# Kernel tuning notes

Measured on AMD Instinct MI355X. Metric: run time of the kernel, lower is better.

## Reference

```python
import jax, jax.numpy as jnp
import numpy as np

N_NODES = 100000
N_EDGES = 3200000
D_FEAT = 256
GC_HID = 20      # CVAEEncoder.hidden_dim default
DEC_HID = 40     # CVAEDecoder.hidden_dim default
Z_DIM = 32
EXPR_DIM = 256
SIGMA_BOUND = 0.0001


def setup_inputs() -> dict:
    key = jax.random.key(0)
    ks = jax.random.split(key, 16)
    inp = {
        "nodes": jax.random.normal(ks[0], (N_NODES, D_FEAT), dtype=jnp.float32),
        "senders": jax.random.randint(ks[1], (N_EDGES,), 0, N_NODES, dtype=jnp.int32),
        "receivers": jax.random.randint(ks[2], (N_EDGES,), 0, N_NODES, dtype=jnp.int32),
        "eps": jax.random.normal(ks[3], (N_NODES, Z_DIM), dtype=jnp.float32),
    }
    def dense(k, fan_in, fan_out):
        # flax default: lecun_normal kernel, zero bias
        w = jax.random.normal(k, (fan_in, fan_out), dtype=jnp.float32) / np.sqrt(fan_in)
        return w, jnp.zeros((fan_out,), jnp.float32)
    inp["W_gc1"], inp["b_gc1"] = dense(ks[4], D_FEAT, GC_HID)
    inp["W_gc2"], inp["b_gc2"] = dense(ks[5], GC_HID, GC_HID)
    inp["W_mu"], inp["b_mu"] = dense(ks[6], GC_HID + D_FEAT, Z_DIM)
    inp["W_ls"], inp["b_ls"] = dense(ks[7], GC_HID + D_FEAT, Z_DIM)
    inp["W_d1"], inp["b_d1"] = dense(ks[8], Z_DIM, DEC_HID)
    inp["W_d2"], inp["b_d2"] = dense(ks[9], DEC_HID, EXPR_DIM)
    return inp


def _gcn_layer(h, senders, receivers, W, b):
    # jraph.GraphConvolution: update_node_fn = softmax(relu(Dense(x))),
    # then symmetric-normalized segment_sum aggregation (no self edges).
    h = jax.nn.softmax(jax.nn.relu(h @ W + b), axis=-1)  # [N, GC_HID]
    ones = jnp.ones(senders.shape, h.dtype)
    deg_s = jax.ops.segment_sum(ones, senders, N_NODES)
    deg_r = jax.ops.segment_sum(ones, receivers, N_NODES)
    h = h * jax.lax.rsqrt(jnp.maximum(deg_s, 1.0))[:, None]
    h = jax.ops.segment_sum(h[senders], receivers, N_NODES)  # irregular gather+scatter
    h = h * jax.lax.rsqrt(jnp.maximum(deg_r, 1.0))[:, None]
    return h


def reference(nodes, senders, receivers, eps,
              W_gc1, b_gc1, W_gc2, b_gc2,
              W_mu, b_mu, W_ls, b_ls,
              W_d1, b_d1, W_d2, b_d2):
    # Encoder: 2 GC layers
    h = _gcn_layer(nodes, senders, receivers, W_gc1, b_gc1)
    h = _gcn_layer(h, senders, receivers, W_gc2, b_gc2)
    h = jnp.concatenate([h, nodes], axis=-1)  # [N, GC_HID + D_FEAT]
    mu = h @ W_mu + b_mu
    logsig2 = h @ W_ls + b_ls
    # Reparameterization
    sigma = SIGMA_BOUND + jnp.exp(0.5 * logsig2)
    z = mu + sigma * eps
    # Decoder MLP (nlayers=2 -> one hidden relu layer)
    d = jax.nn.relu(z @ W_d1 + b_d1)
    Xsample = d @ W_d2 + b_d2
    return Xsample, mu, logsig2
```

## Files before the change

kernel.cpp:

```cpp
#include <hip/hip_runtime.h>
#include <math.h>

#define N_NODES 100000
#define N_EDGES 3200000
#define D_FEAT 256
#define GC_HID 20
#define DEC_HID 40
#define Z_DIM 32

#define EPB 2048
#define NBLK 1563
#define SB 392
#define SBSH 8
#define S2CAP 12288


__device__ inline unsigned short f2bf(float f) {
    unsigned u = __float_as_uint(f);
    return (unsigned short)((u + 0x7FFFu + ((u >> 16) & 1u)) >> 16);
}
__device__ inline float bf2f(unsigned short h) {
    return __uint_as_float((unsigned)h << 16);
}
__device__ inline float bflo(unsigned w) { return __uint_as_float(w << 16); }
__device__ inline float bfhi(unsigned w) { return __uint_as_float(w & 0xFFFF0000u); }

__global__ __launch_bounds__(96) void k_wpack(const float* __restrict__ W1,
                                              const float* __restrict__ Wmu,
                                              const float* __restrict__ Wls,
                                              float* __restrict__ Wp) {
    int k = blockIdx.x, j = threadIdx.x;
    float v = 0.0f;
    if (j < 20) v = W1[k * GC_HID + j];
    else if (j >= 24 && j < 56) v = Wmu[(GC_HID + k) * Z_DIM + (j - 24)];
    else if (j >= 56 && j < 88) v = Wls[(GC_HID + k) * Z_DIM + (j - 56)];
    Wp[k * 96 + j] = v;
}

__global__ __launch_bounds__(512) void k_sort(const int* __restrict__ snd,
                                              const int* __restrict__ rcv,
                                              unsigned* __restrict__ rec_r,
                                              unsigned char* __restrict__ rec_s,
                                              unsigned short* __restrict__ srow_r,
                                              unsigned short* __restrict__ srow_s) {
    __shared__ int es[EPB], er[EPB];
    __shared__ unsigned scan[SB + 1];
    __shared__ unsigned cur[SB];
    __shared__ unsigned sorted[EPB];
    __shared__ unsigned char sorteds[EPB];
    int b = blockIdx.x, t = threadIdx.x;
    int base = b * EPB;
    int cnt = min(EPB, N_EDGES - base);
    for (int i = t; i < cnt; i += 512) { es[i] = snd[base + i]; er[i] = rcv[base + i]; }

    for (int i = t; i < SB + 1; i += 512) scan[i] = 0u;
    __syncthreads();
    for (int i = t; i < cnt; i += 512) atomicAdd(&scan[(er[i] >> SBSH) + 1], 1u);
    __syncthreads();
    for (int off = 1; off < SB + 1; off <<= 1) {
        unsigned v = (t >= off && t < SB + 1) ? scan[t - off] : 0u;
        __syncthreads();
        if (t < SB + 1) scan[t] += v;
        __syncthreads();
    }
    for (int i = t; i < SB + 1; i += 512) srow_r[(size_t)b * (SB + 1) + i] = (unsigned short)scan[i];
    if (t < SB) cur[t] = scan[t];
    __syncthreads();
    for (int i = t; i < cnt; i += 512) {
        int r = er[i];
        unsigned pos = atomicAdd(&cur[r >> SBSH], 1u);
        sorted[pos] = ((unsigned)(r & 255) << 17) | (unsigned)es[i];
    }
    __syncthreads();
    for (int i = t; i < cnt; i += 512) rec_r[(size_t)base + i] = sorted[i];
    __syncthreads();

    for (int i = t; i < SB + 1; i += 512) scan[i] = 0u;
    __syncthreads();
    for (int i = t; i < cnt; i += 512) atomicAdd(&scan[(es[i] >> SBSH) + 1], 1u);
    __syncthreads();
    for (int off = 1; off < SB + 1; off <<= 1) {
        unsigned v = (t >= off && t < SB + 1) ? scan[t - off] : 0u;
        __syncthreads();
        if (t < SB + 1) scan[t] += v;
        __syncthreads();
    }
    for (int i = t; i < SB + 1; i += 512) srow_s[(size_t)b * (SB + 1) + i] = (unsigned short)scan[i];
    if (t < SB) cur[t] = scan[t];
    __syncthreads();
    for (int i = t; i < cnt; i += 512) {
        int s = es[i];
        unsigned pos = atomicAdd(&cur[s >> SBSH], 1u);
        sorteds[pos] = (unsigned char)(s & 255);
    }
    __syncthreads();
    for (int i = t; i < cnt; i += 512) rec_s[(size_t)base + i] = sorteds[i];
}

__global__ __launch_bounds__(512) void k_degs(const unsigned char* __restrict__ rec_s,
                                              const unsigned short* __restrict__ srow_s,
                                              float* __restrict__ rs_s) {
    __shared__ unsigned h[256];
    int s = blockIdx.x, t = threadIdx.x;
    if (t < 256) h[t] = 0u;
    __syncthreads();
    for (int k = t; k < NBLK; k += 512) {
        const unsigned short* row = srow_s + (size_t)k * (SB + 1);
        unsigned st = row[s], en = row[s + 1];
        const unsigned char* rp = rec_s + (size_t)k * EPB;
        for (unsigned i = st; i < en; ++i) atomicAdd(&h[rp[i]], 1u);
    }
    __syncthreads();
    if (t < 256) {
        int n = (s << SBSH) + t;
        if (n < N_NODES) rs_s[n] = rsqrtf(fmaxf((float)h[t], 1.0f));
    }
}

__global__ __launch_bounds__(256) void k_scanB(const unsigned short* __restrict__ srow_r,
                                               unsigned* __restrict__ pref_t,
                                               unsigned* __restrict__ gtot) {
    __shared__ unsigned buf[256];
    int s = blockIdx.x, t = threadIdx.x;
    unsigned run = 0;
    for (int k0 = 0; k0 < NBLK; k0 += 256) {
        int k = k0 + t;
        unsigned v = 0;
        if (k < NBLK) {
            const unsigned short* row = srow_r + (size_t)k * (SB + 1);
            v = (unsigned)row[s + 1] - (unsigned)row[s];
        }
        buf[t] = v;
        __syncthreads();
        for (int off = 1; off < 256; off <<= 1) {
            unsigned x = (t >= off) ? buf[t - off] : 0u;
            __syncthreads();
            buf[t] += x;
            __syncthreads();
        }
        if (k < NBLK) pref_t[(size_t)s * NBLK + k] = run + (buf[t] - v);
        unsigned tot = buf[255];
        __syncthreads();
        run += tot;
    }
    if (t == 0) gtot[s] = run;
}

__global__ __launch_bounds__(512) void k_scanG(const unsigned* __restrict__ gtot,
                                               unsigned* __restrict__ gbase) {
    __shared__ unsigned buf[SB];
    int t = threadIdx.x;
    if (t < SB) buf[t] = gtot[t];
    __syncthreads();
    for (int off = 1; off < SB; off <<= 1) {
        unsigned x = (t >= off && t < SB) ? buf[t - off] : 0u;
        __syncthreads();
        if (t < SB) buf[t] += x;
        __syncthreads();
    }
    if (t < SB) gbase[t + 1] = buf[t];
    if (t == 0) gbase[0] = 0u;
}

__global__ __launch_bounds__(256) void k_gscat(const unsigned* __restrict__ rec_r,
                                               const unsigned short* __restrict__ srow_r,
                                               const unsigned* __restrict__ pref_t,
                                               const unsigned* __restrict__ gbase,
                                               unsigned* __restrict__ grec) {
    __shared__ unsigned recs[EPB];
    __shared__ unsigned short srow[SB + 1];
    int b = blockIdx.x, t = threadIdx.x;
    int base = b * EPB;
    int cnt = min(EPB, N_EDGES - base);
    for (int i = t; i < cnt; i += 256) recs[i] = rec_r[(size_t)base + i];
    for (int i = t; i < SB + 1; i += 256) srow[i] = srow_r[(size_t)b * (SB + 1) + i];
    __syncthreads();
    for (int s = t; s < SB; s += 256) {
        unsigned lo = srow[s], hi = srow[s + 1];
        if (lo == hi) continue;
        unsigned dst = gbase[s] + pref_t[(size_t)s * NBLK + b];
        for (unsigned i = lo; i < hi; ++i) grec[dst + (i - lo)] = recs[i];
    }
}

__global__ __launch_bounds__(256) void k_sort2(unsigned* __restrict__ grec,
                                               const unsigned* __restrict__ gbase,
                                               unsigned* __restrict__ row_ptr) {
    __shared__ unsigned recs[S2CAP];
    __shared__ unsigned hist[256];
    __shared__ unsigned scan[256];
    __shared__ unsigned cur[256];
    int s = blockIdx.x, t = threadIdx.x;
    unsigned lo = gbase[s], hi = gbase[s + 1];
    unsigned cnt = min(hi - lo, (unsigned)S2CAP);
    for (unsigned i = t; i < cnt; i += 256) recs[i] = grec[lo + i];
    hist[t] = 0u;
    __syncthreads();
    for (unsigned i = t; i < cnt; i += 256) atomicAdd(&hist[recs[i] >> 17], 1u);
    __syncthreads();
    unsigned v = hist[t];
    scan[t] = v;
    __syncthreads();
    for (int off = 1; off < 256; off <<= 1) {
        unsigned x = (t >= off) ? scan[t - off] : 0u;
        __syncthreads();
        scan[t] += x;
        __syncthreads();
    }
    unsigned excl = scan[t] - v;
    {
        int n = (s << SBSH) + t;
        if (n <= N_NODES) row_ptr[n] = lo + excl;
    }
    cur[t] = excl;
    __syncthreads();
    for (unsigned i = t; i < cnt; i += 256) {
        unsigned rec = recs[i];
        unsigned pos = atomicAdd(&cur[rec >> 17], 1u);
        grec[lo + pos] = rec & 0x1FFFFu;
    }
}

__global__ __launch_bounds__(320) void k_gg1(const unsigned* __restrict__ row_ptr,
                                             const unsigned* __restrict__ grec,
                                             const unsigned* __restrict__ src,
                                             const float* __restrict__ W2,
                                             const float* __restrict__ b2,
                                             const float* __restrict__ rs_s,
                                             unsigned short* __restrict__ h2_pre) {
    __shared__ float h1[64 * 21];
    __shared__ float Wsh[GC_HID * GC_HID];
    __shared__ float bsh[GC_HID];
    int t = threadIdx.x;
    if (t < GC_HID * GC_HID) Wsh[t] = W2[t];
    if (t >= 400 && t < 400 + GC_HID) bsh[t - 400] = b2[t - 400];
    int nl = t / 5, q = t % 5;
    int node = blockIdx.x * 64 + nl;
    bool live = (node < N_NODES);
    unsigned lo = 0, hi = 0;
    if (live) { lo = row_ptr[node]; hi = row_ptr[node + 1]; }
    float4 a0 = make_float4(0.f, 0.f, 0.f, 0.f);
    float4 a1 = make_float4(0.f, 0.f, 0.f, 0.f);
    float4 a2 = make_float4(0.f, 0.f, 0.f, 0.f);
    float4 a3 = make_float4(0.f, 0.f, 0.f, 0.f);
    const uint2* sp = (const uint2*)src;
    unsigned e = lo;
    for (; e + 4 <= hi; e += 4) {
        unsigned s0 = grec[e], s1 = grec[e + 1], s2 = grec[e + 2], s3 = grec[e + 3];
        uint2 u0 = sp[s0 * 5 + q];
        uint2 u1 = sp[s1 * 5 + q];
        uint2 u2 = sp[s2 * 5 + q];
        uint2 u3 = sp[s3 * 5 + q];
        a0.x += bflo(u0.x); a0.y += bfhi(u0.x); a0.z += bflo(u0.y); a0.w += bfhi(u0.y);
        a1.x += bflo(u1.x); a1.y += bfhi(u1.x); a1.z += bflo(u1.y); a1.w += bfhi(u1.y);
        a2.x += bflo(u2.x); a2.y += bfhi(u2.x); a2.z += bflo(u2.y); a2.w += bfhi(u2.y);
        a3.x += bflo(u3.x); a3.y += bfhi(u3.x); a3.z += bflo(u3.y); a3.w += bfhi(u3.y);
    }
    for (; e < hi; ++e) {
        unsigned s0 = grec[e];
        uint2 u0 = sp[s0 * 5 + q];
        a0.x += bflo(u0.x); a0.y += bfhi(u0.x); a0.z += bflo(u0.y); a0.w += bfhi(u0.y);
    }
    a0.x += a1.x + a2.x + a3.x;
    a0.y += a1.y + a2.y + a3.y;
    a0.z += a1.z + a2.z + a3.z;
    a0.w += a1.w + a2.w + a3.w;
    if (live) {
        float sc = rsqrtf(fmaxf((float)(hi - lo), 1.0f));
        float* row = &h1[nl * 21 + q * 4];
        row[0] = a0.x * sc; row[1] = a0.y * sc;
        row[2] = a0.z * sc; row[3] = a0.w * sc;
    }
    __syncthreads();
    if (t < 64) {
        int nn = blockIdx.x * 64 + t;
        if (nn < N_NODES) {
            float hv[GC_HID];
#pragma unroll
            for (int i = 0; i < GC_HID; ++i) hv[i] = h1[t * 21 + i];
            float o[GC_HID];
#pragma unroll
            for (int j = 0; j < GC_HID; ++j) o[j] = bsh[j];
#pragma unroll
            for (int i = 0; i < GC_HID; ++i) {
                float x = hv[i];
#pragma unroll
                for (int j = 0; j < GC_HID; ++j) o[j] = fmaf(x, Wsh[i * GC_HID + j], o[j]);
            }
            float mx = -1e30f;
#pragma unroll
            for (int j = 0; j < GC_HID; ++j) { o[j] = fmaxf(o[j], 0.0f); mx = fmaxf(mx, o[j]); }
            float s = 0.0f;
#pragma unroll
            for (int j = 0; j < GC_HID; ++j) { o[j] = __expf(o[j] - mx); s += o[j]; }
            float inv = rs_s[nn] / s;
            unsigned pk[10];
#pragma unroll
            for (int i = 0; i < 10; ++i) {
                float v0 = o[2*i] * inv, v1 = o[2*i+1] * inv;
                pk[i] = (unsigned)f2bf(v0) | ((unsigned)f2bf(v1) << 16);
            }
            uint2* op = (uint2*)(h2_pre + (size_t)nn * GC_HID);
#pragma unroll
            for (int i = 0; i < 5; ++i)
                op[i] = make_uint2(pk[2*i], pk[2*i+1]);
        }
    }
}

__global__ __launch_bounds__(512) void k_gg2(const unsigned* __restrict__ row_ptr,
                                             const unsigned* __restrict__ grec,
                                             const unsigned* __restrict__ src,
                                             const unsigned short* __restrict__ pml,
                                             const float* __restrict__ Wmu,
                                             const float* __restrict__ bmu,
                                             const float* __restrict__ Wls,
                                             const float* __restrict__ bls,
                                             float* __restrict__ mu_out,
                                             float* __restrict__ ls_out) {
    __shared__ float h2s[64 * 21];
    int t = threadIdx.x;
    int n0 = blockIdx.x * 64;
    if (t < 320) {
        int nl = t / 5, q = t % 5;
        int node = n0 + nl;
        bool live = (node < N_NODES);
        unsigned lo = 0, hi = 0;
        if (live) { lo = row_ptr[node]; hi = row_ptr[node + 1]; }
        float4 a0 = make_float4(0.f, 0.f, 0.f, 0.f);
        float4 a1 = make_float4(0.f, 0.f, 0.f, 0.f);
        float4 a2 = make_float4(0.f, 0.f, 0.f, 0.f);
        float4 a3 = make_float4(0.f, 0.f, 0.f, 0.f);
        const uint2* sp = (const uint2*)src;
        unsigned e = lo;
        for (; e + 4 <= hi; e += 4) {
            unsigned s0 = grec[e], s1 = grec[e + 1], s2 = grec[e + 2], s3 = grec[e + 3];
            uint2 u0 = sp[s0 * 5 + q];
            uint2 u1 = sp[s1 * 5 + q];
            uint2 u2 = sp[s2 * 5 + q];
            uint2 u3 = sp[s3 * 5 + q];
            a0.x += bflo(u0.x); a0.y += bfhi(u0.x); a0.z += bflo(u0.y); a0.w += bfhi(u0.y);
            a1.x += bflo(u1.x); a1.y += bfhi(u1.x); a1.z += bflo(u1.y); a1.w += bfhi(u1.y);
            a2.x += bflo(u2.x); a2.y += bfhi(u2.x); a2.z += bflo(u2.y); a2.w += bfhi(u2.y);
            a3.x += bflo(u3.x); a3.y += bfhi(u3.x); a3.z += bflo(u3.y); a3.w += bfhi(u3.y);
        }
        for (; e < hi; ++e) {
            unsigned s0 = grec[e];
            uint2 u0 = sp[s0 * 5 + q];
            a0.x += bflo(u0.x); a0.y += bfhi(u0.x); a0.z += bflo(u0.y); a0.w += bfhi(u0.y);
        }
        a0.x += a1.x + a2.x + a3.x;
        a0.y += a1.y + a2.y + a3.y;
        a0.z += a1.z + a2.z + a3.z;
        a0.w += a1.w + a2.w + a3.w;
        if (live) {
            float sc = rsqrtf(fmaxf((float)(hi - lo), 1.0f));
            float* row = &h2s[nl * 21 + q * 4];
            row[0] = a0.x * sc; row[1] = a0.y * sc;
            row[2] = a0.z * sc; row[3] = a0.w * sc;
        }
    }
    __syncthreads();
    int wave = t >> 6, lane = t & 63;
    int og = __builtin_amdgcn_readfirstlane(wave);
    int half = og >> 2;
    int co = (og & 3) << 3;
    int node = n0 + lane;
    if (node >= N_NODES) return;
    const float* W  = half ? Wls : Wmu;
    const float* bb = half ? bls : bmu;
    float* out      = half ? ls_out : mu_out;

    uint4 p = *(const uint4*)(pml + (size_t)node * 64 + half * 32 + co);
    float acc[8];
    acc[0] = bf2f((unsigned short)(p.x & 0xFFFFu));
    acc[1] = bf2f((unsigned short)(p.x >> 16));
    acc[2] = bf2f((unsigned short)(p.y & 0xFFFFu));
    acc[3] = bf2f((unsigned short)(p.y >> 16));
    acc[4] = bf2f((unsigned short)(p.z & 0xFFFFu));
    acc[5] = bf2f((unsigned short)(p.z >> 16));
    acc[6] = bf2f((unsigned short)(p.w & 0xFFFFu));
    acc[7] = bf2f((unsigned short)(p.w >> 16));
#pragma unroll
    for (int j = 0; j < 8; ++j) acc[j] += bb[co + j];

#pragma unroll
    for (int i = 0; i < GC_HID; ++i) {
        float x = h2s[lane * 21 + i];
        const float* wr = W + i * Z_DIM + co;
#pragma unroll
        for (int j = 0; j < 8; ++j) acc[j] = fmaf(x, wr[j], acc[j]);
    }
    float4* op = (float4*)(out + (size_t)node * Z_DIM + co);
    op[0] = make_float4(acc[0], acc[1], acc[2], acc[3]);
    op[1] = make_float4(acc[4], acc[5], acc[6], acc[7]);
}

__global__ __launch_bounds__(256) void k_gc1f(const float* __restrict__ nodes,
                                              const float* __restrict__ Wp,
                                              const float* __restrict__ b1,
                                              const float* __restrict__ rs_s,
                                              unsigned short* __restrict__ h_pre,
                                              unsigned short* __restrict__ pml) {
    __shared__ float tile[2][64 * 33];
    float* gb = &tile[0][0];
    int t = threadIdx.x;
    int g = __builtin_amdgcn_readfirstlane(t >> 6);
    int lane = t & 63;
    int n0 = blockIdx.x * 64;
    int node = n0 + lane;

    {
        int idx = t;
#pragma unroll
        for (int r = 0; r < 2; ++r, idx += 256) {
            int rr = idx >> 3, c4 = idx & 7;
            int gn = n0 + rr;
            float4 v = (gn < N_NODES)
                ? ((const float4*)nodes)[(size_t)gn * 64 + c4]
                : make_float4(0.f, 0.f, 0.f, 0.f);
            float* dst = &tile[0][rr * 33 + c4 * 4];
            dst[0] = v.x; dst[1] = v.y; dst[2] = v.z; dst[3] = v.w;
        }
    }
    __syncthreads();

    float acc[24];
#pragma unroll
    for (int j = 0; j < 24; ++j) acc[j] = 0.0f;

    for (int c = 0; c < 8; ++c) {
        float4 p0, p1;
        if (c < 7) {
            int idx = t, rr = idx >> 3, c4 = idx & 7, gn = n0 + rr;
            p0 = (gn < N_NODES)
                ? ((const float4*)nodes)[(size_t)gn * 64 + (c + 1) * 8 + c4]
                : make_float4(0.f, 0.f, 0.f, 0.f);
            idx = t + 256; rr = idx >> 3; c4 = idx & 7; gn = n0 + rr;
            p1 = (gn < N_NODES)
                ? ((const float4*)nodes)[(size_t)gn * 64 + (c + 1) * 8 + c4]
                : make_float4(0.f, 0.f, 0.f, 0.f);
        }
        const float* trow  = &tile[c & 1][lane * 33];
        const float* wbase = Wp + (size_t)(c * 32) * 96 + g * 24;
#pragma unroll 4
        for (int kk = 0; kk < 32; ++kk) {
            float x = trow[kk];
            const float* wr = wbase + kk * 96;
#pragma unroll
            for (int j = 0; j < 24; ++j) acc[j] = fmaf(x, wr[j], acc[j]);
        }
        if (c < 7) {
            int idx = t, rr = idx >> 3, c4 = idx & 7;
            float* dst = &tile[(c + 1) & 1][rr * 33 + c4 * 4];
            dst[0] = p0.x; dst[1] = p0.y; dst[2] = p0.z; dst[3] = p0.w;
            idx = t + 256; rr = idx >> 3; c4 = idx & 7;
            dst = &tile[(c + 1) & 1][rr * 33 + c4 * 4];
            dst[0] = p1.x; dst[1] = p1.y; dst[2] = p1.z; dst[3] = p1.w;
        }
        __syncthreads();
    }

    if (node < N_NODES) {
        if (g == 0) {
#pragma unroll
            for (int j = 0; j < GC_HID; ++j) gb[lane * 21 + j] = acc[j] + b1[j];
        } else {
            int base = (g - 1) * 24;
            unsigned short* pp = pml + (size_t)node * 64 + base;
            uint4 q0, q1, q2;
            q0.x = (unsigned)f2bf(acc[0]) | ((unsigned)f2bf(acc[1]) << 16);
            q0.y = (unsigned)f2bf(acc[2]) | ((unsigned)f2bf(acc[3]) << 16);
            q0.z = (unsigned)f2bf(acc[4]) | ((unsigned)f2bf(acc[5]) << 16);
            q0.w = (unsigned)f2bf(acc[6]) | ((unsigned)f2bf(acc[7]) << 16);
            q1.x = (unsigned)f2bf(acc[8]) | ((unsigned)f2bf(acc[9]) << 16);
            q1.y = (unsigned)f2bf(acc[10]) | ((unsigned)f2bf(acc[11]) << 16);
            q1.z = (unsigned)f2bf(acc[12]) | ((unsigned)f2bf(acc[13]) << 16);
            q1.w = (unsigned)f2bf(acc[14]) | ((unsigned)f2bf(acc[15]) << 16);
            q2.x = (unsigned)f2bf(acc[16]) | ((unsigned)f2bf(acc[17]) << 16);
            q2.y = (unsigned)f2bf(acc[18]) | ((unsigned)f2bf(acc[19]) << 16);
            q2.z = (unsigned)f2bf(acc[20]) | ((unsigned)f2bf(acc[21]) << 16);
            q2.w = (unsigned)f2bf(acc[22]) | ((unsigned)f2bf(acc[23]) << 16);
            ((uint4*)pp)[0] = q0;
            ((uint4*)pp)[1] = q1;
            if (g != 3) ((uint4*)pp)[2] = q2;
        }
    }
    __syncthreads();
    if (t < 64) {
        int nn = n0 + t;
        if (nn < N_NODES) {
            float v[GC_HID];
            float mx = -1e30f;
#pragma unroll
            for (int j = 0; j < GC_HID; ++j) {
                v[j] = fmaxf(gb[t * 21 + j], 0.0f);
                mx = fmaxf(mx, v[j]);
            }
            float s = 0.0f;
#pragma unroll
            for (int j = 0; j < GC_HID; ++j) {
                v[j] = __expf(v[j] - mx);
                s += v[j];
            }
            float inv = rs_s[nn] / s;
            unsigned pk[10];
#pragma unroll
            for (int i = 0; i < 10; ++i) {
                float v0 = v[2*i] * inv, v1 = v[2*i+1] * inv;
                pk[i] = (unsigned)f2bf(v0) | ((unsigned)f2bf(v1) << 16);
            }
            uint2* op = (uint2*)(h_pre + (size_t)nn * GC_HID);
#pragma unroll
            for (int i = 0; i < 5; ++i)
                op[i] = make_uint2(pk[2*i], pk[2*i+1]);
        }
    }
}

__global__ __launch_bounds__(512) void k_dec(const float* __restrict__ mu,
                                             const float* __restrict__ ls,
                                             const float* __restrict__ eps,
                                             const float* __restrict__ Wd1,
                                             const float* __restrict__ bd1,
                                             const float* __restrict__ Wd2,
                                             const float* __restrict__ bd2,
                                             float* __restrict__ X) {
    __shared__ float ds[128 * 41];
    int t = threadIdx.x;
    int wave = t >> 6, lane = t & 63;
    int n0 = blockIdx.x * 128;
    {
        int wu = __builtin_amdgcn_readfirstlane(wave);
        int qd = wu & 3;
        int nh = wu >> 2;
        int nrow = nh * 64 + lane;
        int node = n0 + nrow;
        if (node < N_NODES) {
            float z[Z_DIM];
            const float4* mp = (const float4*)(mu + (size_t)node * Z_DIM);
            const float4* lp = (const float4*)(ls + (size_t)node * Z_DIM);
            const float4* ep = (const float4*)(eps + (size_t)node * Z_DIM);
#pragma unroll
            for (int v = 0; v < Z_DIM / 4; ++v) {
                float4 m = mp[v], l = lp[v], e = ep[v];
                z[4*v+0] = m.x + (1e-4f + __expf(0.5f * l.x)) * e.x;
                z[4*v+1] = m.y + (1e-4f + __expf(0.5f * l.y)) * e.y;
                z[4*v+2] = m.z + (1e-4f + __expf(0.5f * l.z)) * e.z;
                z[4*v+3] = m.w + (1e-4f + __expf(0.5f * l.w)) * e.w;
            }
            float d[10];
#pragma unroll
            for (int j = 0; j < 10; ++j) d[j] = bd1[qd * 10 + j];
#pragma unroll
            for (int i = 0; i < Z_DIM; ++i) {
                float x = z[i];
                const float* wr = Wd1 + i * DEC_HID + qd * 10;
#pragma unroll
                for (int j = 0; j < 10; ++j) d[j] = fmaf(x, wr[j], d[j]);
            }
            float* dst = &ds[nrow * 41 + qd * 10];
#pragma unroll
            for (int j = 0; j < 10; ++j) dst[j] = fmaxf(d[j], 0.0f);
        }
    }
    __syncthreads();
#pragma unroll
    for (int p = 0; p < 2; ++p) {
        int ch = __builtin_amdgcn_readfirstlane(wave >> 1) + p * 4;
        int nrow = (wave & 1) * 64 + lane;
        int node = n0 + nrow;
        if (node < N_NODES) {
            int co = ch << 5;
            float o[32];
#pragma unroll
            for (int j = 0; j < 32; ++j) o[j] = bd2[co + j];
            const float* drow = &ds[nrow * 41];
#pragma unroll 8
            for (int k = 0; k < DEC_HID; ++k) {
                float x = drow[k];
                const float* wr = Wd2 + k * D_FEAT + co;
#pragma unroll
                for (int j = 0; j < 32; ++j) o[j] = fmaf(x, wr[j], o[j]);
            }
            float4* xp = (float4*)(X + (size_t)node * D_FEAT + co);
#pragma unroll
            for (int v = 0; v < 8; ++v)
                xp[v] = make_float4(o[4*v], o[4*v+1], o[4*v+2], o[4*v+3]);
        }
    }
}

extern "C" void kernel_launch(void* const* d_in, const int* in_sizes, int n_in,
                              void* d_out, int out_size, void* d_ws, size_t ws_size,
                              hipStream_t stream) {
    const float* nodes = (const float*)d_in[0];
    const int*   snd   = (const int*)d_in[1];
    const int*   rcv   = (const int*)d_in[2];
    const float* eps   = (const float*)d_in[3];
    const float* W1    = (const float*)d_in[4];
    const float* b1    = (const float*)d_in[5];
    const float* W2    = (const float*)d_in[6];
    const float* b2    = (const float*)d_in[7];
    const float* Wmu   = (const float*)d_in[8];
    const float* bmu   = (const float*)d_in[9];
    const float* Wls   = (const float*)d_in[10];
    const float* bls   = (const float*)d_in[11];
    const float* Wd1   = (const float*)d_in[12];
    const float* bd1   = (const float*)d_in[13];
    const float* Wd2   = (const float*)d_in[14];
    const float* bd2   = (const float*)d_in[15];

    char* ws = (char*)d_ws;
    unsigned short* h_pre    = (unsigned short*)(ws);
    unsigned short* agg      = (unsigned short*)(ws + 8000000);
    unsigned*       grec     = (unsigned*)(ws + 16000000);
    unsigned*       rec_r    = (unsigned*)(ws + 28804096);
    unsigned short* pml      = (unsigned short*)(ws + 28804096);
    unsigned short* srow_r   = (unsigned short*)(ws + 41608192);
    unsigned*       pref_t   = (unsigned*)(ws + 42836720);
    unsigned*       row_ptr  = (unsigned*)(ws + 45287504);
    unsigned*       gtot     = (unsigned*)(ws + 45687508);
    unsigned*       gbase    = (unsigned*)(ws + 45689076);
    float*          rs_s     = (float*)(ws + 45690648);
    unsigned char*  rec_s    = (unsigned char*)(ws + 46090648);
    unsigned short* srow_s   = (unsigned short*)(ws + 49291672);
    float*          Wpack    = (float*)(ws + 50520192);

    float* X      = (float*)d_out;
    float* mu_out = X + (size_t)N_NODES * D_FEAT;
    float* ls_out = mu_out + (size_t)N_NODES * Z_DIM;

    k_wpack<<<256, 96, 0, stream>>>(W1, Wmu, Wls, Wpack);
    k_sort<<<NBLK, 512, 0, stream>>>(snd, rcv, rec_r, rec_s, srow_r, srow_s);
    k_degs<<<SB, 512, 0, stream>>>(rec_s, srow_s, rs_s);
    k_scanB<<<SB, 256, 0, stream>>>(srow_r, pref_t, gtot);
    k_scanG<<<1, 512, 0, stream>>>(gtot, gbase);
    k_gscat<<<NBLK, 256, 0, stream>>>(rec_r, srow_r, pref_t, gbase, grec);
    k_sort2<<<SB, 256, 0, stream>>>(grec, gbase, row_ptr);

    k_gc1f<<<1563, 256, 0, stream>>>(nodes, Wpack, b1, rs_s, h_pre, pml);
    k_gg1<<<1563, 320, 0, stream>>>(row_ptr, grec, (const unsigned*)h_pre,
                                    W2, b2, rs_s, agg);
    k_gg2<<<1563, 512, 0, stream>>>(row_ptr, grec, (const unsigned*)agg, pml,
                                    Wmu, bmu, Wls, bls, mu_out, ls_out);
    k_dec<<<782, 512, 0, stream>>>(mu_out, ls_out, eps, Wd1, bd1, Wd2, bd2, X);
}
```

Before: 354.5 us.

## Replace local receiver sort with histogram plus direct atomic scatter into buckets

The first pass now only builds per-block receiver-bucket histograms instead of locally sorting packed records and writing them out. A second kernel rereads senders and receivers and scatters each record straight into its global bucket position using shared-memory atomic cursors. This removes the intermediate rec_r write and read and the local sort stage, at the cost of reading the edge arrays twice. Order within a bucket becomes nondeterministic, which the later per-bucket sort (k_sort2) is expected to handle.

```diff
diff --git a/kernel.cpp b/kernel.cpp
--- a/kernel.cpp
+++ b/kernel.cpp
@@ -37,48 +37,30 @@
     Wp[k * 96 + j] = v;
 }
 
-__global__ __launch_bounds__(512) void k_sort(const int* __restrict__ snd,
+__global__ __launch_bounds__(512) void k_hist(const int* __restrict__ snd,
                                               const int* __restrict__ rcv,
-                                              unsigned* __restrict__ rec_r,
                                               unsigned char* __restrict__ rec_s,
-                                              unsigned short* __restrict__ srow_r,
+                                              unsigned short* __restrict__ cnt_r,
                                               unsigned short* __restrict__ srow_s) {
-    __shared__ int es[EPB], er[EPB];
+    __shared__ int es[EPB];
+    __shared__ unsigned hist[SB];
     __shared__ unsigned scan[SB + 1];
     __shared__ unsigned cur[SB];
-    __shared__ unsigned sorted[EPB];
     __shared__ unsigned char sorteds[EPB];
     int b = blockIdx.x, t = threadIdx.x;
     int base = b * EPB;
     int cnt = min(EPB, N_EDGES - base);
-    for (int i = t; i < cnt; i += 512) { es[i] = snd[base + i]; er[i] = rcv[base + i]; }
-
+    for (int i = t; i < cnt; i += 512) es[i] = snd[base + i];
+    for (int i = t; i < SB; i += 512) hist[i] = 0u;
     for (int i = t; i < SB + 1; i += 512) scan[i] = 0u;
     __syncthreads();
-    for (int i = t; i < cnt; i += 512) atomicAdd(&scan[(er[i] >> SBSH) + 1], 1u);
-    __syncthreads();
-    for (int off = 1; off < SB + 1; off <<= 1) {
-        unsigned v = (t >= off && t < SB + 1) ? scan[t - off] : 0u;
-        __syncthreads();
-        if (t < SB + 1) scan[t] += v;
-        __syncthreads();
-    }
-    for (int i = t; i < SB + 1; i += 512) srow_r[(size_t)b * (SB + 1) + i] = (unsigned short)scan[i];
-    if (t < SB) cur[t] = scan[t];
-    __syncthreads();
     for (int i = t; i < cnt; i += 512) {
-        int r = er[i];
-        unsigned pos = atomicAdd(&cur[r >> SBSH], 1u);
-        sorted[pos] = ((unsigned)(r & 255) << 17) | (unsigned)es[i];
-    }
-    __syncthreads();
-    for (int i = t; i < cnt; i += 512) rec_r[(size_t)base + i] = sorted[i];
-    __syncthreads();
-
-    for (int i = t; i < SB + 1; i += 512) scan[i] = 0u;
-    __syncthreads();
-    for (int i = t; i < cnt; i += 512) atomicAdd(&scan[(es[i] >> SBSH) + 1], 1u);
-    __syncthreads();
+        atomicAdd(&hist[rcv[base + i] >> SBSH], 1u);
+        atomicAdd(&scan[(es[i] >> SBSH) + 1], 1u);
+    }
+    __syncthreads();
+    for (int i = t; i < SB; i += 512)
+        cnt_r[(size_t)b * SB + i] = (unsigned short)hist[i];
     for (int off = 1; off < SB + 1; off <<= 1) {
         unsigned v = (t >= off && t < SB + 1) ? scan[t - off] : 0u;
         __syncthreads();
@@ -117,7 +99,7 @@
     }
 }
 
-__global__ __launch_bounds__(256) void k_scanB(const unsigned short* __restrict__ srow_r,
+__global__ __launch_bounds__(256) void k_scanB(const unsigned short* __restrict__ cnt_r,
                                                unsigned* __restrict__ pref_t,
                                                unsigned* __restrict__ gtot) {
     __shared__ unsigned buf[256];
@@ -125,11 +107,7 @@
     unsigned run = 0;
     for (int k0 = 0; k0 < NBLK; k0 += 256) {
         int k = k0 + t;
-        unsigned v = 0;
-        if (k < NBLK) {
-            const unsigned short* row = srow_r + (size_t)k * (SB + 1);
-            v = (unsigned)row[s + 1] - (unsigned)row[s];
-        }
+        unsigned v = (k < NBLK) ? (unsigned)cnt_r[(size_t)k * SB + s] : 0u;
         buf[t] = v;
         __syncthreads();
         for (int off = 1; off < 256; off <<= 1) {
@@ -162,24 +140,23 @@
     if (t == 0) gbase[0] = 0u;
 }
 
-__global__ __launch_bounds__(256) void k_gscat(const unsigned* __restrict__ rec_r,
-                                               const unsigned short* __restrict__ srow_r,
+__global__ __launch_bounds__(256) void k_scat2(const int* __restrict__ snd,
+                                               const int* __restrict__ rcv,
                                                const unsigned* __restrict__ pref_t,
                                                const unsigned* __restrict__ gbase,
                                                unsigned* __restrict__ grec) {
-    __shared__ unsigned recs[EPB];
-    __shared__ unsigned short srow[SB + 1];
+    __shared__ unsigned cur2[SB];
     int b = blockIdx.x, t = threadIdx.x;
+    for (int s = t; s < SB; s += 256)
+        cur2[s] = gbase[s] + pref_t[(size_t)s * NBLK + b];
+    __syncthreads();
     int base = b * EPB;
     int cnt = min(EPB, N_EDGES - base);
-    for (int i = t; i < cnt; i += 256) recs[i] = rec_r[(size_t)base + i];
-    for (int i = t; i < SB + 1; i += 256) srow[i] = srow_r[(size_t)b * (SB + 1) + i];
-    __syncthreads();
-    for (int s = t; s < SB; s += 256) {
-        unsigned lo = srow[s], hi = srow[s + 1];
-        if (lo == hi) continue;
-        unsigned dst = gbase[s] + pref_t[(size_t)s * NBLK + b];
-        for (unsigned i = lo; i < hi; ++i) grec[dst + (i - lo)] = recs[i];
+    for (int i = t; i < cnt; i += 256) {
+        int r = rcv[base + i];
+        int s = snd[base + i];
+        unsigned idx = atomicAdd(&cur2[r >> SBSH], 1u);
+        grec[idx] = ((unsigned)(r & 255) << 17) | (unsigned)s;
     }
 }
 
@@ -615,9 +592,8 @@
     unsigned short* h_pre    = (unsigned short*)(ws);
     unsigned short* agg      = (unsigned short*)(ws + 8000000);
     unsigned*       grec     = (unsigned*)(ws + 16000000);
-    unsigned*       rec_r    = (unsigned*)(ws + 28804096);
     unsigned short* pml      = (unsigned short*)(ws + 28804096);
-    unsigned short* srow_r   = (unsigned short*)(ws + 41608192);
+    unsigned short* cnt_r    = (unsigned short*)(ws + 41608192);
     unsigned*       pref_t   = (unsigned*)(ws + 42836720);
     unsigned*       row_ptr  = (unsigned*)(ws + 45287504);
     unsigned*       gtot     = (unsigned*)(ws + 45687508);
@@ -632,11 +608,11 @@
     float* ls_out = mu_out + (size_t)N_NODES * Z_DIM;
 
     k_wpack<<<256, 96, 0, stream>>>(W1, Wmu, Wls, Wpack);
-    k_sort<<<NBLK, 512, 0, stream>>>(snd, rcv, rec_r, rec_s, srow_r, srow_s);
+    k_hist<<<NBLK, 512, 0, stream>>>(snd, rcv, rec_s, cnt_r, srow_s);
     k_degs<<<SB, 512, 0, stream>>>(rec_s, srow_s, rs_s);
-    k_scanB<<<SB, 256, 0, stream>>>(srow_r, pref_t, gtot);
+    k_scanB<<<SB, 256, 0, stream>>>(cnt_r, pref_t, gtot);
     k_scanG<<<1, 512, 0, stream>>>(gtot, gbase);
-    k_gscat<<<NBLK, 256, 0, stream>>>(rec_r, srow_r, pref_t, gbase, grec);
+    k_scat2<<<NBLK, 256, 0, stream>>>(snd, rcv, pref_t, gbase, grec);
     k_sort2<<<SB, 256, 0, stream>>>(grec, gbase, row_ptr);
 
     k_gc1f<<<1563, 256, 0, stream>>>(nodes, Wpack, b1, rs_s, h_pre, pml);
```

After: 363.9 us. 2.7% more time.
